# Optimization experiments

Hardware: AMD Instinct MI355X
Metric: run time of the kernel (lower is better)

## Reference

```python
import jax, jax.numpy as jnp
import numpy as np

RETRIEVAL_SHARPNESS = 50.0
TWO_PI = 2.0 * np.pi


def setup_inputs() -> dict:
    key = jax.random.key(0)
    k1, k2, k3, k4 = jax.random.split(key, 4)
    W, S = 4096, 4096
    return {
        "hologram_re": jax.random.normal(k1, (W, S), dtype=jnp.float32),
        "hologram_im": jax.random.normal(k2, (W, S), dtype=jnp.float32),
        "cue_re": jax.random.normal(k3, (W, S), dtype=jnp.float32),
        "cue_im": jax.random.normal(k4, (W, S), dtype=jnp.float32),
        "n_keys": 1024,
    }


def _make_keys(n_keys, W):
    # write(): key_idx -> exp(1j * arange(W) * (idx+1)*2pi/W), stacked [N, W]
    freqs = (jnp.arange(n_keys, dtype=jnp.float32) + 1.0) * (TWO_PI / W)  # [N]
    phase = freqs[:, None] * jnp.arange(W, dtype=jnp.float32)[None, :]    # [N, W]
    return jnp.exp(1j * phase)  # complex64 [N, W]


def reference(hologram_re, hologram_im, cue_re, cue_im, n_keys):
    W, S = hologram_re.shape
    holo = hologram_re + 1j * hologram_im  # [W, S] complex64
    cue = cue_re + 1j * cue_im             # [W, S] complex64
    keys = _make_keys(n_keys, W)            # [N, W]

    # noisy_mix = (hologram * cue.conj()).sum(dim=1) -> [W]
    noisy_mix = jnp.sum(holo * jnp.conj(cue), axis=1)
    # correlations = |dot(noisy_mix, k)| per key (torch.dot: no conjugation)
    correlations = jnp.abs(keys @ noisy_mix)  # [N]
    attention = jax.nn.softmax(correlations * RETRIEVAL_SHARPNESS)  # [N]
    # clean_key = sum_k attention[k] * keys[k] -> [W]
    clean_key = attention.astype(keys.dtype) @ keys
    out = holo * clean_key[:, None]  # [W, S] complex64
    return jnp.stack([out.real, out.imag])  # [2, W, S] float32
```

## Files before the change

### kernel.cpp

```cpp
#include <hip/hip_runtime.h>
#include <math.h>

#define W 4096
#define S 4096
#define NK_MAX 1024

typedef float v4f __attribute__((ext_vector_type(4)));


__global__ void nm_kernel(const float* __restrict__ hr, const float* __restrict__ hi,
                          const float* __restrict__ cr, const float* __restrict__ ci,
                          float2* __restrict__ nm, float2* __restrict__ table) {
    int w = blockIdx.x;
    int t = threadIdx.x;
    size_t base = (size_t)w * 1024;
    const v4f* hr4 = (const v4f*)hr;
    const v4f* hi4 = (const v4f*)hi;
    const v4f* cr4 = (const v4f*)cr;
    const v4f* ci4 = (const v4f*)ci;

    v4f a[4], b[4], c[4], d[4];
#pragma unroll
    for (int k = 0; k < 4; k++) {
        size_t i = base + t + k * 256;
        a[k] = hr4[i];
        b[k] = hi4[i];
        c[k] = __builtin_nontemporal_load(&cr4[i]);
        d[k] = __builtin_nontemporal_load(&ci4[i]);
    }

    if (t == 0) {
        double theta = (double)w * (6.283185307179586 / (double)W);
        table[w] = make_float2((float)cos(theta), (float)sin(theta));
    }

    v4f vr = {0.f, 0.f, 0.f, 0.f}, vi = {0.f, 0.f, 0.f, 0.f};
#pragma unroll
    for (int k = 0; k < 4; k++) {
        vr += a[k] * c[k] + b[k] * d[k];
        vi += b[k] * c[k] - a[k] * d[k];
    }
    float sr = vr.x + vr.y + vr.z + vr.w;
    float si = vi.x + vi.y + vi.z + vi.w;

    for (int off = 32; off; off >>= 1) {
        sr += __shfl_down(sr, off);
        si += __shfl_down(si, off);
    }
    __shared__ float s0[4], s1[4];
    int lane = t & 63, wid = t >> 6;
    if (lane == 0) { s0[wid] = sr; s1[wid] = si; }
    __syncthreads();
    if (t == 0) {
        nm[w] = make_float2(s0[0] + s0[1] + s0[2] + s0[3],
                            s1[0] + s1[1] + s1[2] + s1[3]);
    }
}

__global__ void corr_kernel(const float2* __restrict__ nm, const float2* __restrict__ table,
                            float* __restrict__ corr, const int* __restrict__ nkp) {
    int n = blockIdx.x;
    if (n >= *nkp) return;
    int f = n + 1;
    float sr = 0.f, si = 0.f;
    for (int w = threadIdx.x; w < W; w += 256) {
        int idx = (w * f) & (W - 1);
        float2 t = table[idx];
        float2 v = nm[w];
        sr += t.x * v.x - t.y * v.y;
        si += t.x * v.y + t.y * v.x;
    }
    for (int off = 32; off; off >>= 1) {
        sr += __shfl_down(sr, off);
        si += __shfl_down(si, off);
    }
    __shared__ float s0[4], s1[4];
    int lane = threadIdx.x & 63, wid = threadIdx.x >> 6;
    if (lane == 0) { s0[wid] = sr; s1[wid] = si; }
    __syncthreads();
    if (threadIdx.x == 0) {
        float r = s0[0] + s0[1] + s0[2] + s0[3];
        float m = s1[0] + s1[1] + s1[2] + s1[3];
        corr[n] = sqrtf(r * r + m * m);
    }
}

__global__ void out_kernel(const float* __restrict__ hr, const float* __restrict__ hi,
                           const float* __restrict__ corr, const float2* __restrict__ table,
                           const int* __restrict__ nkp, float* __restrict__ out) {
    int w = blockIdx.x;
    int t = threadIdx.x;
    size_t base = (size_t)w * 1024;
    const size_t total4 = (size_t)W * S / 4;
    int lane = t & 63, wid = t >> 6;
    __shared__ float red[8];

    v4f a[4], b[4];
#pragma unroll
    for (int k = 0; k < 4; k++) {
        size_t i = base + t + k * 256;
        a[k] = ((const v4f*)hr)[i];
        b[k] = ((const v4f*)hi)[i];
    }

    int nk = *nkp;

    float v[4];
    float vmax = -INFINITY;
#pragma unroll
    for (int j = 0; j < 4; j++) {
        int i = t + j * 256;
        v[j] = (i < nk) ? corr[i] * 50.0f : -INFINITY;
        vmax = fmaxf(vmax, v[j]);
    }
    for (int off = 32; off; off >>= 1) vmax = fmaxf(vmax, __shfl_down(vmax, off));
    if (lane == 0) red[wid] = vmax;
    __syncthreads();
    float M = fmaxf(fmaxf(red[0], red[1]), fmaxf(red[2], red[3]));

    float e[4];
    float esum = 0.f;
#pragma unroll
    for (int j = 0; j < 4; j++) {
        int i = t + j * 256;
        e[j] = (i < nk) ? expf(v[j] - M) : 0.f;
        esum += e[j];
    }
    for (int off = 32; off; off >>= 1) esum += __shfl_down(esum, off);
    if (lane == 0) red[4 + wid] = esum;
    __syncthreads();
    float SUM = red[4] + red[5] + red[6] + red[7];
    __syncthreads();

    float crr = 0.f, cii = 0.f;
#pragma unroll
    for (int j = 0; j < 4; j++) {
        int i = t + j * 256;
        if (i < nk) {
            int idx = (w * (i + 1)) & (W - 1);
            float2 tt = table[idx];
            crr += e[j] * tt.x;
            cii += e[j] * tt.y;
        }
    }
    for (int off = 32; off; off >>= 1) {
        crr += __shfl_down(crr, off);
        cii += __shfl_down(cii, off);
    }
    if (lane == 0) { red[wid] = crr; red[4 + wid] = cii; }
    __syncthreads();
    float ckr = (red[0] + red[1] + red[2] + red[3]) / SUM;
    float cki = (red[4] + red[5] + red[6] + red[7]) / SUM;

#pragma unroll
    for (int k = 0; k < 4; k++) {
        size_t i = base + t + k * 256;
        v4f re = a[k] * ckr - b[k] * cki;
        v4f im = a[k] * cki + b[k] * ckr;
        __builtin_nontemporal_store(re, &((v4f*)out)[i]);
        __builtin_nontemporal_store(im, &((v4f*)out)[i + total4]);
    }
}

extern "C" void kernel_launch(void* const* d_in, const int* in_sizes, int n_in,
                              void* d_out, int out_size, void* d_ws, size_t ws_size,
                              hipStream_t stream) {
    const float* hr = (const float*)d_in[0];
    const float* hi = (const float*)d_in[1];
    const float* cr = (const float*)d_in[2];
    const float* ci = (const float*)d_in[3];
    const int* nk = (const int*)d_in[4];

    float* ws = (float*)d_ws;
    float2* table = (float2*)ws;
    float2* nm    = (float2*)(ws + 8192);
    float* corr   = ws + 16384;
    float* out = (float*)d_out;

    nm_kernel<<<W, 256, 0, stream>>>(hr, hi, cr, ci, nm, table);
    corr_kernel<<<NK_MAX, 256, 0, stream>>>(nm, table, corr, nk);
    out_kernel<<<W, 256, 0, stream>>>(hr, hi, corr, table, nk, out);
}
```

Before: 337.0 us.

## Fuse three stages into one cooperative kernel with grid-wide syncs

Replaces the three separate launches with a single cooperative kernel of 1024 blocks, one wave per row, using grid.sync between the noisy-mix, correlation and output stages. Each block computes the softmax weights into shared memory once and reuses them for its four rows. The aim is to remove launch gaps and the tail idle time between kernels, and possibly to get L2 reuse of hologram rows. The cost is grid-sync overhead, fewer resident waves available to hide memory latency, and re-reading hr/hi in the last stage, which may no longer be cached. If the cooperative launch fails, the code falls back to the old three-kernel path.

```diff
diff --git a/kernel.cpp b/kernel.cpp
--- a/kernel.cpp
+++ b/kernel.cpp
@@ -1,12 +1,170 @@
 #include <hip/hip_runtime.h>
+#include <hip/hip_cooperative_groups.h>
 #include <math.h>
+
+namespace cg = cooperative_groups;
 
 #define W 4096
 #define S 4096
 #define NK_MAX 1024
+#define NBLK 1024
 
 typedef float v4f __attribute__((ext_vector_type(4)));
 
+
+__global__ __launch_bounds__(256, 4) void fused_kernel(
+    const float* __restrict__ hr, const float* __restrict__ hi,
+    const float* __restrict__ cr, const float* __restrict__ ci,
+    const int* __restrict__ nkp,
+    float2* __restrict__ table, float2* __restrict__ nm,
+    float* __restrict__ corr, float* __restrict__ out)
+{
+    cg::grid_group grid = cg::this_grid();
+    const int bid = blockIdx.x;
+    const int t = threadIdx.x;
+    const int lane = t & 63, wid = t >> 6;
+
+    __shared__ float s0[4], s1[4];
+    __shared__ float red[8];
+    __shared__ float satt[NK_MAX];
+
+    const v4f* hr4 = (const v4f*)hr;
+    const v4f* hi4 = (const v4f*)hi;
+    const v4f* cr4 = (const v4f*)cr;
+    const v4f* ci4 = (const v4f*)ci;
+
+    if (t < 4) {
+        int k = bid * 4 + t;
+        double theta = (double)k * (6.283185307179586 / (double)W);
+        table[k] = make_float2((float)cos(theta), (float)sin(theta));
+    }
+
+    {
+        int w = bid * 4 + wid;
+        size_t base = (size_t)w * 1024;
+        v4f vr = {0.f, 0.f, 0.f, 0.f}, vi = {0.f, 0.f, 0.f, 0.f};
+#pragma unroll 1
+        for (int ch = 0; ch < 4; ch++) {
+            v4f a[4], b[4], c[4], d[4];
+#pragma unroll
+            for (int k = 0; k < 4; k++) {
+                size_t i = base + ch * 256 + k * 64 + lane;
+                a[k] = hr4[i];
+                b[k] = hi4[i];
+                c[k] = __builtin_nontemporal_load(&cr4[i]);
+                d[k] = __builtin_nontemporal_load(&ci4[i]);
+            }
+#pragma unroll
+            for (int k = 0; k < 4; k++) {
+                vr += a[k] * c[k] + b[k] * d[k];
+                vi += b[k] * c[k] - a[k] * d[k];
+            }
+        }
+        float sr = vr.x + vr.y + vr.z + vr.w;
+        float si = vi.x + vi.y + vi.z + vi.w;
+        for (int off = 32; off; off >>= 1) {
+            sr += __shfl_down(sr, off);
+            si += __shfl_down(si, off);
+        }
+        if (lane == 0) nm[w] = make_float2(sr, si);
+    }
+
+    grid.sync();
+
+    int nk = *nkp;
+    if (bid < nk) {
+        int f = bid + 1;
+        float sr = 0.f, si = 0.f;
+        for (int w = t; w < W; w += 256) {
+            int idx = (w * f) & (W - 1);
+            float2 tt = table[idx];
+            float2 v = nm[w];
+            sr += tt.x * v.x - tt.y * v.y;
+            si += tt.x * v.y + tt.y * v.x;
+        }
+        for (int off = 32; off; off >>= 1) {
+            sr += __shfl_down(sr, off);
+            si += __shfl_down(si, off);
+        }
+        if (lane == 0) { s0[wid] = sr; s1[wid] = si; }
+        __syncthreads();
+        if (t == 0) {
+            float r = s0[0] + s0[1] + s0[2] + s0[3];
+            float m = s1[0] + s1[1] + s1[2] + s1[3];
+            corr[bid] = sqrtf(r * r + m * m);
+        }
+    }
+
+    grid.sync();
+
+    float v[4];
+    float vmax = -INFINITY;
+#pragma unroll
+    for (int j = 0; j < 4; j++) {
+        int i = t + j * 256;
+        v[j] = (i < nk) ? corr[i] * 50.0f : -INFINITY;
+        vmax = fmaxf(vmax, v[j]);
+    }
+    for (int off = 32; off; off >>= 1) vmax = fmaxf(vmax, __shfl_down(vmax, off));
+    if (lane == 0) red[wid] = vmax;
+    __syncthreads();
+    float M = fmaxf(fmaxf(red[0], red[1]), fmaxf(red[2], red[3]));
+
+    float esum = 0.f;
+#pragma unroll
+    for (int j = 0; j < 4; j++) {
+        int i = t + j * 256;
+        float e = (i < nk) ? expf(v[j] - M) : 0.f;
+        satt[i] = e;
+        esum += e;
+    }
+    for (int off = 32; off; off >>= 1) esum += __shfl_down(esum, off);
+    if (lane == 0) red[4 + wid] = esum;
+    __syncthreads();
+    float SUM = red[4] + red[5] + red[6] + red[7];
+
+    {
+        int w = bid * 4 + wid;
+        size_t base = (size_t)w * 1024;
+        const size_t total4 = (size_t)W * S / 4;
+
+        float crr = 0.f, cii = 0.f;
+#pragma unroll 4
+        for (int k = 0; k < 16; k++) {
+            int n = lane + k * 64;
+            int idx = (w * (n + 1)) & (W - 1);
+            float2 tt = table[idx];
+            float a = satt[n];
+            crr += a * tt.x;
+            cii += a * tt.y;
+        }
+        for (int off = 32; off; off >>= 1) {
+            crr += __shfl_down(crr, off);
+            cii += __shfl_down(cii, off);
+        }
+        float ckr = __shfl(crr, 0) / SUM;
+        float cki = __shfl(cii, 0) / SUM;
+
+#pragma unroll 1
+        for (int ch = 0; ch < 4; ch++) {
+            v4f a[4], b[4];
+#pragma unroll
+            for (int k = 0; k < 4; k++) {
+                size_t i = base + ch * 256 + k * 64 + lane;
+                a[k] = hr4[i];
+                b[k] = hi4[i];
+            }
+#pragma unroll
+            for (int k = 0; k < 4; k++) {
+                size_t i = base + ch * 256 + k * 64 + lane;
+                v4f re = a[k] * ckr - b[k] * cki;
+                v4f im = a[k] * cki + b[k] * ckr;
+                __builtin_nontemporal_store(re, &((v4f*)out)[i]);
+                __builtin_nontemporal_store(im, &((v4f*)out)[i + total4]);
+            }
+        }
+    }
+}
 
 __global__ void nm_kernel(const float* __restrict__ hr, const float* __restrict__ hi,
                           const float* __restrict__ cr, const float* __restrict__ ci,
@@ -28,13 +186,11 @@
         c[k] = __builtin_nontemporal_load(&cr4[i]);
         d[k] = __builtin_nontemporal_load(&ci4[i]);
     }
-
     if (t == 0) {
         double theta = (double)w * (6.283185307179586 / (double)W);
         table[w] = make_float2((float)cos(theta), (float)sin(theta));
     }
-
-    v4f vr = {0.f, 0.f, 0.f, 0.f}, vi = {0.f, 0.f, 0.f, 0.f};
+    v4f vr = {0.f,0.f,0.f,0.f}, vi = {0.f,0.f,0.f,0.f};
 #pragma unroll
     for (int k = 0; k < 4; k++) {
         vr += a[k] * c[k] + b[k] * d[k];
@@ -42,7 +198,6 @@
     }
     float sr = vr.x + vr.y + vr.z + vr.w;
     float si = vi.x + vi.y + vi.z + vi.w;
-
     for (int off = 32; off; off >>= 1) {
         sr += __shfl_down(sr, off);
         si += __shfl_down(si, off);
@@ -51,10 +206,8 @@
     int lane = t & 63, wid = t >> 6;
     if (lane == 0) { s0[wid] = sr; s1[wid] = si; }
     __syncthreads();
-    if (t == 0) {
-        nm[w] = make_float2(s0[0] + s0[1] + s0[2] + s0[3],
-                            s1[0] + s1[1] + s1[2] + s1[3]);
-    }
+    if (t == 0)
+        nm[w] = make_float2(s0[0]+s0[1]+s0[2]+s0[3], s1[0]+s1[1]+s1[2]+s1[3]);
 }
 
 __global__ void corr_kernel(const float2* __restrict__ nm, const float2* __restrict__ table,
@@ -102,7 +255,6 @@
         a[k] = ((const v4f*)hr)[i];
         b[k] = ((const v4f*)hi)[i];
     }
-
     int nk = *nkp;
 
     float v[4];
@@ -177,7 +329,13 @@
     float* corr   = ws + 16384;
     float* out = (float*)d_out;
 
-    nm_kernel<<<W, 256, 0, stream>>>(hr, hi, cr, ci, nm, table);
-    corr_kernel<<<NK_MAX, 256, 0, stream>>>(nm, table, corr, nk);
-    out_kernel<<<W, 256, 0, stream>>>(hr, hi, corr, table, nk, out);
-}
+    void* args[] = { (void*)&hr, (void*)&hi, (void*)&cr, (void*)&ci, (void*)&nk,
+                     (void*)&table, (void*)&nm, (void*)&corr, (void*)&out };
+    hipError_t err = hipLaunchCooperativeKernel((const void*)fused_kernel,
+                                                dim3(NBLK), dim3(256), args, 0, stream);
+    if (err != hipSuccess) {
+        nm_kernel<<<W, 256, 0, stream>>>(hr, hi, cr, ci, nm, table);
+        corr_kernel<<<NK_MAX, 256, 0, stream>>>(nm, table, corr, nk);
+        out_kernel<<<W, 256, 0, stream>>>(hr, hi, corr, table, nk, out);
+    }
+}
```

Measured after the change: 583.6 us. 1.73x slower.

## Map one wavefront per hologram row and amortize softmax across four rows

Applied to the files above, without the earlier changes.

Each block now handles four rows, one per wavefront, so the row reductions need only wave shuffles and no shared-memory barrier. In the output kernel the softmax over correlations is computed once per block and stored in shared memory, so four rows share it instead of redoing it per row. Each wavefront then computes its own clean-key coefficient over all keys. Loads are issued in four sequential chunks instead of all at once, which lowers the number of bytes in flight per wave and may hurt latency hiding on this bandwidth-bound workload.

```diff
diff --git a/kernel.cpp b/kernel.cpp
--- a/kernel.cpp
+++ b/kernel.cpp
@@ -11,50 +11,48 @@
 __global__ void nm_kernel(const float* __restrict__ hr, const float* __restrict__ hi,
                           const float* __restrict__ cr, const float* __restrict__ ci,
                           float2* __restrict__ nm, float2* __restrict__ table) {
-    int w = blockIdx.x;
     int t = threadIdx.x;
-    size_t base = (size_t)w * 1024;
+    int lane = t & 63, wid = t >> 6;
+    int bid = blockIdx.x;
     const v4f* hr4 = (const v4f*)hr;
     const v4f* hi4 = (const v4f*)hi;
     const v4f* cr4 = (const v4f*)cr;
     const v4f* ci4 = (const v4f*)ci;
 
-    v4f a[4], b[4], c[4], d[4];
-#pragma unroll
-    for (int k = 0; k < 4; k++) {
-        size_t i = base + t + k * 256;
-        a[k] = hr4[i];
-        b[k] = hi4[i];
-        c[k] = __builtin_nontemporal_load(&cr4[i]);
-        d[k] = __builtin_nontemporal_load(&ci4[i]);
+    if (t < 4) {
+        int k = bid * 4 + t;
+        double theta = (double)k * (6.283185307179586 / (double)W);
+        table[k] = make_float2((float)cos(theta), (float)sin(theta));
     }
 
-    if (t == 0) {
-        double theta = (double)w * (6.283185307179586 / (double)W);
-        table[w] = make_float2((float)cos(theta), (float)sin(theta));
-    }
+    int w = bid * 4 + wid;
+    size_t base = (size_t)w * 1024;
 
     v4f vr = {0.f, 0.f, 0.f, 0.f}, vi = {0.f, 0.f, 0.f, 0.f};
+#pragma unroll 1
+    for (int ch = 0; ch < 4; ch++) {
+        v4f a[4], b[4], c[4], d[4];
 #pragma unroll
-    for (int k = 0; k < 4; k++) {
-        vr += a[k] * c[k] + b[k] * d[k];
-        vi += b[k] * c[k] - a[k] * d[k];
+        for (int k = 0; k < 4; k++) {
+            size_t i = base + ch * 256 + k * 64 + lane;
+            a[k] = hr4[i];
+            b[k] = hi4[i];
+            c[k] = __builtin_nontemporal_load(&cr4[i]);
+            d[k] = __builtin_nontemporal_load(&ci4[i]);
+        }
+#pragma unroll
+        for (int k = 0; k < 4; k++) {
+            vr += a[k] * c[k] + b[k] * d[k];
+            vi += b[k] * c[k] - a[k] * d[k];
+        }
     }
     float sr = vr.x + vr.y + vr.z + vr.w;
     float si = vi.x + vi.y + vi.z + vi.w;
-
     for (int off = 32; off; off >>= 1) {
         sr += __shfl_down(sr, off);
         si += __shfl_down(si, off);
     }
-    __shared__ float s0[4], s1[4];
-    int lane = t & 63, wid = t >> 6;
-    if (lane == 0) { s0[wid] = sr; s1[wid] = si; }
-    __syncthreads();
-    if (t == 0) {
-        nm[w] = make_float2(s0[0] + s0[1] + s0[2] + s0[3],
-                            s1[0] + s1[1] + s1[2] + s1[3]);
-    }
+    if (lane == 0) nm[w] = make_float2(sr, si);
 }
 
 __global__ void corr_kernel(const float2* __restrict__ nm, const float2* __restrict__ table,
@@ -88,22 +86,14 @@
 __global__ void out_kernel(const float* __restrict__ hr, const float* __restrict__ hi,
                            const float* __restrict__ corr, const float2* __restrict__ table,
                            const int* __restrict__ nkp, float* __restrict__ out) {
-    int w = blockIdx.x;
+    __shared__ float satt[NK_MAX];
+    __shared__ float red[8];
     int t = threadIdx.x;
-    size_t base = (size_t)w * 1024;
-    const size_t total4 = (size_t)W * S / 4;
     int lane = t & 63, wid = t >> 6;
-    __shared__ float red[8];
-
-    v4f a[4], b[4];
-#pragma unroll
-    for (int k = 0; k < 4; k++) {
-        size_t i = base + t + k * 256;
-        a[k] = ((const v4f*)hr)[i];
-        b[k] = ((const v4f*)hi)[i];
-    }
-
+    int bid = blockIdx.x;
     int nk = *nkp;
+    const v4f* hr4 = (const v4f*)hr;
+    const v4f* hi4 = (const v4f*)hi;
 
     float v[4];
     float vmax = -INFINITY;
@@ -118,47 +108,57 @@
     __syncthreads();
     float M = fmaxf(fmaxf(red[0], red[1]), fmaxf(red[2], red[3]));
 
-    float e[4];
     float esum = 0.f;
 #pragma unroll
     for (int j = 0; j < 4; j++) {
         int i = t + j * 256;
-        e[j] = (i < nk) ? expf(v[j] - M) : 0.f;
-        esum += e[j];
+        float e = (i < nk) ? expf(v[j] - M) : 0.f;
+        satt[i] = e;
+        esum += e;
     }
     for (int off = 32; off; off >>= 1) esum += __shfl_down(esum, off);
     if (lane == 0) red[4 + wid] = esum;
     __syncthreads();
     float SUM = red[4] + red[5] + red[6] + red[7];
-    __syncthreads();
+
+    int w = bid * 4 + wid;
+    size_t base = (size_t)w * 1024;
+    const size_t total4 = (size_t)W * S / 4;
 
     float crr = 0.f, cii = 0.f;
-#pragma unroll
-    for (int j = 0; j < 4; j++) {
-        int i = t + j * 256;
-        if (i < nk) {
-            int idx = (w * (i + 1)) & (W - 1);
-            float2 tt = table[idx];
-            crr += e[j] * tt.x;
-            cii += e[j] * tt.y;
-        }
+#pragma unroll 4
+    for (int k = 0; k < 16; k++) {
+        int n = lane + k * 64;
+        int idx = (w * (n + 1)) & (W - 1);
+        float2 tt = table[idx];
+        float a = satt[n];
+        crr += a * tt.x;
+        cii += a * tt.y;
     }
     for (int off = 32; off; off >>= 1) {
         crr += __shfl_down(crr, off);
         cii += __shfl_down(cii, off);
     }
-    if (lane == 0) { red[wid] = crr; red[4 + wid] = cii; }
-    __syncthreads();
-    float ckr = (red[0] + red[1] + red[2] + red[3]) / SUM;
-    float cki = (red[4] + red[5] + red[6] + red[7]) / SUM;
+    float ckr = __shfl(crr, 0) / SUM;
+    float cki = __shfl(cii, 0) / SUM;
 
+#pragma unroll 1
+    for (int ch = 0; ch < 4; ch++) {
+        v4f a[4], b[4];
 #pragma unroll
-    for (int k = 0; k < 4; k++) {
-        size_t i = base + t + k * 256;
-        v4f re = a[k] * ckr - b[k] * cki;
-        v4f im = a[k] * cki + b[k] * ckr;
-        __builtin_nontemporal_store(re, &((v4f*)out)[i]);
-        __builtin_nontemporal_store(im, &((v4f*)out)[i + total4]);
+        for (int k = 0; k < 4; k++) {
+            size_t i = base + ch * 256 + k * 64 + lane;
+            a[k] = hr4[i];
+            b[k] = hi4[i];
+        }
+#pragma unroll
+        for (int k = 0; k < 4; k++) {
+            size_t i = base + ch * 256 + k * 64 + lane;
+            v4f re = a[k] * ckr - b[k] * cki;
+            v4f im = a[k] * cki + b[k] * ckr;
+            __builtin_nontemporal_store(re, &((v4f*)out)[i]);
+            __builtin_nontemporal_store(im, &((v4f*)out)[i + total4]);
+        }
     }
 }
 
@@ -177,7 +177,7 @@
     float* corr   = ws + 16384;
     float* out = (float*)d_out;
 
-    nm_kernel<<<W, 256, 0, stream>>>(hr, hi, cr, ci, nm, table);
+    nm_kernel<<<W / 4, 256, 0, stream>>>(hr, hi, cr, ci, nm, table);
     corr_kernel<<<NK_MAX, 256, 0, stream>>>(nm, table, corr, nk);
-    out_kernel<<<W, 256, 0, stream>>>(hr, hi, corr, table, nk, out);
+    out_kernel<<<W / 4, 256, 0, stream>>>(hr, hi, corr, table, nk, out);
 }
```

After: 346.5 us. +2.8%, slower.
